# Performance work log

Measured on AMD Instinct MI355X. Metric: run time of the kernel, lower is better.

Reference implementation:

```python
import jax, jax.numpy as jnp
import numpy as np

LN_EPS = 1e-5


def setup_inputs() -> dict:
    key = jax.random.key(0)
    k1, k2, k3, k4 = jax.random.split(key, 4)
    N, D, E = 10000, 512, 150000
    scale = 1.0 / np.sqrt(D)
    return {
        "node_feature": jax.random.normal(k1, (N, D), dtype=jnp.float32),
        "edge_index": jax.random.randint(k2, (2, E), 0, N, dtype=jnp.int64),
        "ln_gamma": jnp.ones((D,), dtype=jnp.float32),
        "ln_beta": jnp.zeros((D,), dtype=jnp.float32),
        "w_l": jax.random.normal(k3, (D, D), dtype=jnp.float32) * scale,
        "b_l": jnp.zeros((D,), dtype=jnp.float32),
        "w_r": jax.random.normal(k4, (D, D), dtype=jnp.float32) * scale,
    }


def reference(node_feature, edge_index, ln_gamma, ln_beta, w_l, b_l, w_r):
    N = node_feature.shape[0]
    residual = node_feature

    # LayerNorm over feature dim
    mu = jnp.mean(node_feature, axis=-1, keepdims=True)
    var = jnp.mean(jnp.square(node_feature - mu), axis=-1, keepdims=True)
    x = (node_feature - mu) * jax.lax.rsqrt(var + LN_EPS) * ln_gamma + ln_beta

    # SAGEConv (mean aggr): gather x_j from src, segment-mean into dst
    src, dst = edge_index[0], edge_index[1]
    msg = x[src]                                   # [E, D]
    summed = jax.ops.segment_sum(msg, dst, num_segments=N)        # [N, D]
    cnt = jax.ops.segment_sum(jnp.ones_like(dst, dtype=x.dtype), dst, num_segments=N)
    agg = summed / jnp.maximum(cnt, 1.0)[:, None]

    # out = lin_l(agg) + lin_r(x)  (lin_r has no bias in PyG SAGEConv)
    out = agg @ w_l.T + b_l + x @ w_r.T
    out = jax.nn.relu(out)
    # dropout is identity in eval mode
    return out + residual
```

## Files before the change

### kernel.cpp

```cpp
#include <hip/hip_runtime.h>
#include <hip/hip_bf16.h>

typedef float f32x4 __attribute__((ext_vector_type(4)));
typedef __bf16 bf16x8 __attribute__((ext_vector_type(8)));
typedef unsigned short u16x8 __attribute__((ext_vector_type(8)));

#define N_NODES 10000
#define DIM 512
#define MPAD 10112
#define DEGCAP 96

__global__ __launch_bounds__(256) void zero_kernel(int* __restrict__ cnt) {
    cnt[blockIdx.x * 256 + threadIdx.x] = 0;
}

__global__ __launch_bounds__(256) void phase1_kernel(
    const float* __restrict__ wl, const float* __restrict__ wr,
    __hip_bfloat16* __restrict__ W,
    const float* __restrict__ xin, const float* __restrict__ gamma,
    const float* __restrict__ beta, __hip_bfloat16* __restrict__ A,
    const int* __restrict__ eidx, int* __restrict__ cnt, int* __restrict__ adj,
    int E, int fill_start) {
    int b = blockIdx.x;
    int tid = threadIdx.x;

    if (b < 512) {
        int idx = b * 256 + tid;
        int base = idx * 4;
        int d = base >> 10;
        int k = base & 1023;
        const float* src = (k < 512) ? (wl + d * 512 + k) : (wr + d * 512 + (k - 512));
        float4 v = *(const float4*)src;
        __hip_bfloat16* o = W + (size_t)d * 1024 + k;
        o[0] = __float2bfloat16(v.x);
        o[1] = __float2bfloat16(v.y);
        o[2] = __float2bfloat16(v.z);
        o[3] = __float2bfloat16(v.w);
    } else if (b < fill_start) {
        int row = (b - 512) * 4 + (tid >> 6);
        int lane = tid & 63;
        const float* xr = xin + (size_t)row * DIM + lane * 8;
        float4 v0 = *(const float4*)xr;
        float4 v1 = *(const float4*)(xr + 4);
        float s  = v0.x + v0.y + v0.z + v0.w + v1.x + v1.y + v1.z + v1.w;
        float ss = v0.x*v0.x + v0.y*v0.y + v0.z*v0.z + v0.w*v0.w
                 + v1.x*v1.x + v1.y*v1.y + v1.z*v1.z + v1.w*v1.w;
        #pragma unroll
        for (int o = 32; o > 0; o >>= 1) {
            s  += __shfl_xor(s, o, 64);
            ss += __shfl_xor(ss, o, 64);
        }
        float mu  = s * (1.0f / 512.0f);
        float var = ss * (1.0f / 512.0f) - mu * mu;
        float rstd = rsqrtf(var + 1e-5f);
        float4 g0 = *(const float4*)(gamma + lane * 8);
        float4 g1 = *(const float4*)(gamma + lane * 8 + 4);
        float4 b0 = *(const float4*)(beta + lane * 8);
        float4 b1 = *(const float4*)(beta + lane * 8 + 4);
        __hip_bfloat16* a = A + (size_t)row * 1024 + 512 + lane * 8;
        a[0] = __float2bfloat16((v0.x - mu) * rstd * g0.x + b0.x);
        a[1] = __float2bfloat16((v0.y - mu) * rstd * g0.y + b0.y);
        a[2] = __float2bfloat16((v0.z - mu) * rstd * g0.z + b0.z);
        a[3] = __float2bfloat16((v0.w - mu) * rstd * g0.w + b0.w);
        a[4] = __float2bfloat16((v1.x - mu) * rstd * g1.x + b1.x);
        a[5] = __float2bfloat16((v1.y - mu) * rstd * g1.y + b1.y);
        a[6] = __float2bfloat16((v1.z - mu) * rstd * g1.z + b1.z);
        a[7] = __float2bfloat16((v1.w - mu) * rstd * g1.w + b1.w);
    } else {
        int i = (b - fill_start) * 256 + tid;
        if (i < E) {
            int dst = eidx[E + i];
            int src = eidx[i];
            int pos = atomicAdd(&cnt[dst], 1);
            if (pos < DEGCAP) adj[dst * DEGCAP + pos] = src;
        }
    }
}

__global__ __launch_bounds__(256) void gather_kernel(const int* __restrict__ cnt,
                                                     const int* __restrict__ adj,
                                                     __hip_bfloat16* __restrict__ A) {
    int gw = (blockIdx.x * 256 + threadIdx.x) >> 6;
    int lane = threadIdx.x & 63;
    int deg = cnt[gw];
    const int* al = adj + gw * DEGCAP;
    float acc0[8] = {}, acc1[8] = {};
    int j = 0;
    for (; j + 8 <= deg; j += 8) {
        int a0 = al[j], a1 = al[j+1], a2 = al[j+2], a3 = al[j+3];
        int a4 = al[j+4], a5 = al[j+5], a6 = al[j+6], a7 = al[j+7];
        u16x8 v0 = *(const u16x8*)(A + (size_t)a0 * 1024 + 512 + lane * 8);
        u16x8 v1 = *(const u16x8*)(A + (size_t)a1 * 1024 + 512 + lane * 8);
        u16x8 v2 = *(const u16x8*)(A + (size_t)a2 * 1024 + 512 + lane * 8);
        u16x8 v3 = *(const u16x8*)(A + (size_t)a3 * 1024 + 512 + lane * 8);
        u16x8 v4 = *(const u16x8*)(A + (size_t)a4 * 1024 + 512 + lane * 8);
        u16x8 v5 = *(const u16x8*)(A + (size_t)a5 * 1024 + 512 + lane * 8);
        u16x8 v6 = *(const u16x8*)(A + (size_t)a6 * 1024 + 512 + lane * 8);
        u16x8 v7 = *(const u16x8*)(A + (size_t)a7 * 1024 + 512 + lane * 8);
        #pragma unroll
        for (int k = 0; k < 8; ++k) {
            acc0[k] += __uint_as_float((unsigned)v0[k] << 16)
                     + __uint_as_float((unsigned)v1[k] << 16)
                     + __uint_as_float((unsigned)v2[k] << 16)
                     + __uint_as_float((unsigned)v3[k] << 16);
            acc1[k] += __uint_as_float((unsigned)v4[k] << 16)
                     + __uint_as_float((unsigned)v5[k] << 16)
                     + __uint_as_float((unsigned)v6[k] << 16)
                     + __uint_as_float((unsigned)v7[k] << 16);
        }
    }
    for (; j + 4 <= deg; j += 4) {
        int a0 = al[j], a1 = al[j+1], a2 = al[j+2], a3 = al[j+3];
        u16x8 v0 = *(const u16x8*)(A + (size_t)a0 * 1024 + 512 + lane * 8);
        u16x8 v1 = *(const u16x8*)(A + (size_t)a1 * 1024 + 512 + lane * 8);
        u16x8 v2 = *(const u16x8*)(A + (size_t)a2 * 1024 + 512 + lane * 8);
        u16x8 v3 = *(const u16x8*)(A + (size_t)a3 * 1024 + 512 + lane * 8);
        #pragma unroll
        for (int k = 0; k < 8; ++k) {
            acc0[k] += __uint_as_float((unsigned)v0[k] << 16)
                     + __uint_as_float((unsigned)v1[k] << 16);
            acc1[k] += __uint_as_float((unsigned)v2[k] << 16)
                     + __uint_as_float((unsigned)v3[k] << 16);
        }
    }
    for (; j < deg; ++j) {
        int a0 = al[j];
        u16x8 v0 = *(const u16x8*)(A + (size_t)a0 * 1024 + 512 + lane * 8);
        #pragma unroll
        for (int k = 0; k < 8; ++k)
            acc0[k] += __uint_as_float((unsigned)v0[k] << 16);
    }
    float sc = 1.0f / fmaxf((float)deg, 1.0f);
    __hip_bfloat16* o = A + (size_t)gw * 1024 + lane * 8;
    #pragma unroll
    for (int k = 0; k < 8; ++k)
        o[k] = __float2bfloat16((acc0[k] + acc1[k]) * sc);
}

__global__ __launch_bounds__(256) void gemm_kernel(const __hip_bfloat16* __restrict__ A,
                                                   const __hip_bfloat16* __restrict__ Wb,
                                                   const float* __restrict__ bias,
                                                   const float* __restrict__ resid,
                                                   float* __restrict__ out) {
    __shared__ __hip_bfloat16 As[3][64 * 32];
    __shared__ __hip_bfloat16 Bs[3][64 * 32];
    const int tid = threadIdx.x;
    const int lane = tid & 63;
    const int w = tid >> 6;
    const int wr = w >> 1, wc = w & 1;

    int bid = blockIdx.x;
    int tl = (bid & 7) * 158 + (bid >> 3);
    int mx = tl >> 3, ny = tl & 7;
    const size_t arow0 = (size_t)mx * 64;
    const size_t bcol0 = (size_t)ny * 64;

    f32x4 acc[2][2] = {};

    const int rsw = ((lane & 15) >> 1) & 3;
    const int csw = (((lane >> 4) ^ rsw) & 3) * 8;

#define STAGE(buf, t)                                                                \
    {                                                                                \
        int r = tid >> 2, sl = tid & 3;                                              \
        int c8 = sl ^ ((r >> 1) & 3);                                                \
        const __hip_bfloat16* ga = A + (size_t)(arow0 + r) * 1024 + (t) * 32 + c8 * 8; \
        __builtin_amdgcn_global_load_lds(                                            \
            (const __attribute__((address_space(1))) void*)ga,                       \
            (__attribute__((address_space(3))) void*)(As[buf] + tid * 8), 16, 0, 0); \
        const __hip_bfloat16* gb = Wb + (size_t)(bcol0 + r) * 1024 + (t) * 32 + c8 * 8; \
        __builtin_amdgcn_global_load_lds(                                            \
            (const __attribute__((address_space(1))) void*)gb,                       \
            (__attribute__((address_space(3))) void*)(Bs[buf] + tid * 8), 16, 0, 0); \
    }

    STAGE(0, 0)
    STAGE(1, 1)

    #pragma unroll
    for (int t = 0; t < 32; ++t) {
        if (t < 31) { asm volatile("s_waitcnt vmcnt(2)" ::: "memory"); }
        else        { asm volatile("s_waitcnt vmcnt(0)" ::: "memory"); }
        __builtin_amdgcn_s_barrier();
        __builtin_amdgcn_sched_barrier(0);
        if (t + 2 < 32) STAGE((t + 2) % 3, t + 2)

        const int p = t % 3;
        bf16x8 af[2], bfr[2];
        #pragma unroll
        for (int m = 0; m < 2; ++m)
            af[m] = *(const bf16x8*)(As[p] + (wr * 32 + m * 16 + (lane & 15)) * 32 + csw);
        #pragma unroll
        for (int n = 0; n < 2; ++n)
            bfr[n] = *(const bf16x8*)(Bs[p] + (wc * 32 + n * 16 + (lane & 15)) * 32 + csw);
        #pragma unroll
        for (int m = 0; m < 2; ++m)
            #pragma unroll
            for (int n = 0; n < 2; ++n)
                acc[m][n] = __builtin_amdgcn_mfma_f32_16x16x32_bf16(af[m], bfr[n], acc[m][n], 0, 0, 0);
    }
#undef STAGE

    #pragma unroll
    for (int m = 0; m < 2; ++m) {
        int rowb = (int)arow0 + wr * 32 + m * 16 + (lane >> 4) * 4;
        #pragma unroll
        for (int n = 0; n < 2; ++n) {
            int col = (int)bcol0 + wc * 32 + n * 16 + (lane & 15);
            float bv = bias[col];
            #pragma unroll
            for (int j = 0; j < 4; ++j) {
                int row = rowb + j;
                if (row < N_NODES) {
                    float v = acc[m][n][j] + bv;
                    v = v > 0.0f ? v : 0.0f;
                    out[(size_t)row * 512 + col] = v + resid[(size_t)row * 512 + col];
                }
            }
        }
    }
}

extern "C" void kernel_launch(void* const* d_in, const int* in_sizes, int n_in,
                              void* d_out, int out_size, void* d_ws, size_t ws_size,
                              hipStream_t stream) {
    const float* node  = (const float*)d_in[0];
    const int*   eidx  = (const int*)d_in[1];
    const float* gamma = (const float*)d_in[2];
    const float* beta  = (const float*)d_in[3];
    const float* wl    = (const float*)d_in[4];
    const float* bl    = (const float*)d_in[5];
    const float* wr    = (const float*)d_in[6];
    float* out = (float*)d_out;
    const int E = in_sizes[1] / 2;

    char* ws = (char*)d_ws;
    int* cnt = (int*)ws;
    int* adj = cnt + 10240;
    size_t adj_bytes = ((size_t)N_NODES * DEGCAP * 4 + 255) & ~(size_t)255;
    __hip_bfloat16* A = (__hip_bfloat16*)((char*)adj + adj_bytes);
    __hip_bfloat16* W = (__hip_bfloat16*)((char*)A + (size_t)MPAD * 1024 * 2);

    const int fill_start = 512 + 2500;
    const int nFill = (E + 255) / 256;

    zero_kernel<<<40, 256, 0, stream>>>(cnt);
    phase1_kernel<<<fill_start + nFill, 256, 0, stream>>>(
        wl, wr, W, node, gamma, beta, A, eidx, cnt, adj, E, fill_start);
    gather_kernel<<<(N_NODES * 64) / 256, 256, 0, stream>>>(cnt, adj, A);
    gemm_kernel<<<1264, 256, 0, stream>>>(A, W, bl, node, out);
}
```

Measured before the change: 70.16 us.

## Partition gather feature columns by XCC with persistent atomic work queues

The gather kernel now reads the hardware XCC id and assigns each of four XCC groups a 128-column quarter of the normalized features. Blocks pull 4-node chunks from a per-quarter atomic queue, so each XCC's L2 only holds its own column slice of the feature table. The idea is to raise L2 hit rates for the random neighbour gathers and to balance uneven degrees through dynamic scheduling. In exchange each lane now does narrower 4-byte loads, each adjacency list is read four times, and the scheme relies on the XCC id mapping (xcc&3 on an 8-XCC part) and on an atomic counter per chunk.

```diff
diff --git a/kernel.cpp b/kernel.cpp
--- a/kernel.cpp
+++ b/kernel.cpp
@@ -79,62 +79,68 @@
 
 __global__ __launch_bounds__(256) void gather_kernel(const int* __restrict__ cnt,
                                                      const int* __restrict__ adj,
-                                                     __hip_bfloat16* __restrict__ A) {
-    int gw = (blockIdx.x * 256 + threadIdx.x) >> 6;
-    int lane = threadIdx.x & 63;
-    int deg = cnt[gw];
-    const int* al = adj + gw * DEGCAP;
-    float acc0[8] = {}, acc1[8] = {};
-    int j = 0;
-    for (; j + 8 <= deg; j += 8) {
-        int a0 = al[j], a1 = al[j+1], a2 = al[j+2], a3 = al[j+3];
-        int a4 = al[j+4], a5 = al[j+5], a6 = al[j+6], a7 = al[j+7];
-        u16x8 v0 = *(const u16x8*)(A + (size_t)a0 * 1024 + 512 + lane * 8);
-        u16x8 v1 = *(const u16x8*)(A + (size_t)a1 * 1024 + 512 + lane * 8);
-        u16x8 v2 = *(const u16x8*)(A + (size_t)a2 * 1024 + 512 + lane * 8);
-        u16x8 v3 = *(const u16x8*)(A + (size_t)a3 * 1024 + 512 + lane * 8);
-        u16x8 v4 = *(const u16x8*)(A + (size_t)a4 * 1024 + 512 + lane * 8);
-        u16x8 v5 = *(const u16x8*)(A + (size_t)a5 * 1024 + 512 + lane * 8);
-        u16x8 v6 = *(const u16x8*)(A + (size_t)a6 * 1024 + 512 + lane * 8);
-        u16x8 v7 = *(const u16x8*)(A + (size_t)a7 * 1024 + 512 + lane * 8);
-        #pragma unroll
-        for (int k = 0; k < 8; ++k) {
-            acc0[k] += __uint_as_float((unsigned)v0[k] << 16)
-                     + __uint_as_float((unsigned)v1[k] << 16)
-                     + __uint_as_float((unsigned)v2[k] << 16)
-                     + __uint_as_float((unsigned)v3[k] << 16);
-            acc1[k] += __uint_as_float((unsigned)v4[k] << 16)
-                     + __uint_as_float((unsigned)v5[k] << 16)
-                     + __uint_as_float((unsigned)v6[k] << 16)
-                     + __uint_as_float((unsigned)v7[k] << 16);
-        }
-    }
-    for (; j + 4 <= deg; j += 4) {
-        int a0 = al[j], a1 = al[j+1], a2 = al[j+2], a3 = al[j+3];
-        u16x8 v0 = *(const u16x8*)(A + (size_t)a0 * 1024 + 512 + lane * 8);
-        u16x8 v1 = *(const u16x8*)(A + (size_t)a1 * 1024 + 512 + lane * 8);
-        u16x8 v2 = *(const u16x8*)(A + (size_t)a2 * 1024 + 512 + lane * 8);
-        u16x8 v3 = *(const u16x8*)(A + (size_t)a3 * 1024 + 512 + lane * 8);
-        #pragma unroll
-        for (int k = 0; k < 8; ++k) {
-            acc0[k] += __uint_as_float((unsigned)v0[k] << 16)
-                     + __uint_as_float((unsigned)v1[k] << 16);
-            acc1[k] += __uint_as_float((unsigned)v2[k] << 16)
-                     + __uint_as_float((unsigned)v3[k] << 16);
-        }
-    }
-    for (; j < deg; ++j) {
-        int a0 = al[j];
-        u16x8 v0 = *(const u16x8*)(A + (size_t)a0 * 1024 + 512 + lane * 8);
-        #pragma unroll
-        for (int k = 0; k < 8; ++k)
-            acc0[k] += __uint_as_float((unsigned)v0[k] << 16);
-    }
-    float sc = 1.0f / fmaxf((float)deg, 1.0f);
-    __hip_bfloat16* o = A + (size_t)gw * 1024 + lane * 8;
-    #pragma unroll
-    for (int k = 0; k < 8; ++k)
-        o[k] = __float2bfloat16((acc0[k] + acc1[k]) * sc);
+                                                     __hip_bfloat16* __restrict__ A,
+                                                     int* __restrict__ queues) {
+    int xcc;
+    asm volatile("s_getreg_b32 %0, hwreg(HW_REG_XCC_ID)" : "=s"(xcc));
+    const int q = xcc & 3;
+    const int w = threadIdx.x >> 6;
+    const int lane = threadIdx.x & 63;
+    const char* xbase = (const char*)A + 1024 + (size_t)q * 256 + lane * 4;
+    __shared__ int chunk_s;
+
+    for (;;) {
+        if (threadIdx.x == 0) chunk_s = atomicAdd(&queues[q], 1);
+        __syncthreads();
+        int chunk = chunk_s;
+        __syncthreads();
+        if (chunk >= 2500) break;
+        int node = chunk * 4 + w;
+        int deg = cnt[node];
+        const int* al = adj + node * DEGCAP;
+        float a0 = 0.f, a1 = 0.f;
+        int j = 0;
+        for (; j + 8 <= deg; j += 8) {
+            int n0 = al[j],   n1 = al[j+1], n2 = al[j+2], n3 = al[j+3];
+            int n4 = al[j+4], n5 = al[j+5], n6 = al[j+6], n7 = al[j+7];
+            unsigned v0 = *(const unsigned*)(xbase + (size_t)n0 * 2048);
+            unsigned v1 = *(const unsigned*)(xbase + (size_t)n1 * 2048);
+            unsigned v2 = *(const unsigned*)(xbase + (size_t)n2 * 2048);
+            unsigned v3 = *(const unsigned*)(xbase + (size_t)n3 * 2048);
+            unsigned v4 = *(const unsigned*)(xbase + (size_t)n4 * 2048);
+            unsigned v5 = *(const unsigned*)(xbase + (size_t)n5 * 2048);
+            unsigned v6 = *(const unsigned*)(xbase + (size_t)n6 * 2048);
+            unsigned v7 = *(const unsigned*)(xbase + (size_t)n7 * 2048);
+            a0 += __uint_as_float(v0 << 16) + __uint_as_float(v1 << 16)
+                + __uint_as_float(v2 << 16) + __uint_as_float(v3 << 16)
+                + __uint_as_float(v4 << 16) + __uint_as_float(v5 << 16)
+                + __uint_as_float(v6 << 16) + __uint_as_float(v7 << 16);
+            a1 += __uint_as_float(v0 & 0xffff0000u) + __uint_as_float(v1 & 0xffff0000u)
+                + __uint_as_float(v2 & 0xffff0000u) + __uint_as_float(v3 & 0xffff0000u)
+                + __uint_as_float(v4 & 0xffff0000u) + __uint_as_float(v5 & 0xffff0000u)
+                + __uint_as_float(v6 & 0xffff0000u) + __uint_as_float(v7 & 0xffff0000u);
+        }
+        for (; j + 4 <= deg; j += 4) {
+            int n0 = al[j], n1 = al[j+1], n2 = al[j+2], n3 = al[j+3];
+            unsigned v0 = *(const unsigned*)(xbase + (size_t)n0 * 2048);
+            unsigned v1 = *(const unsigned*)(xbase + (size_t)n1 * 2048);
+            unsigned v2 = *(const unsigned*)(xbase + (size_t)n2 * 2048);
+            unsigned v3 = *(const unsigned*)(xbase + (size_t)n3 * 2048);
+            a0 += __uint_as_float(v0 << 16) + __uint_as_float(v1 << 16)
+                + __uint_as_float(v2 << 16) + __uint_as_float(v3 << 16);
+            a1 += __uint_as_float(v0 & 0xffff0000u) + __uint_as_float(v1 & 0xffff0000u)
+                + __uint_as_float(v2 & 0xffff0000u) + __uint_as_float(v3 & 0xffff0000u);
+        }
+        for (; j < deg; ++j) {
+            unsigned v0 = *(const unsigned*)(xbase + (size_t)al[j] * 2048);
+            a0 += __uint_as_float(v0 << 16);
+            a1 += __uint_as_float(v0 & 0xffff0000u);
+        }
+        float sc = 1.0f / fmaxf((float)deg, 1.0f);
+        __hip_bfloat16* o = (__hip_bfloat16*)((char*)A + (size_t)node * 2048 + (size_t)q * 256 + lane * 4);
+        o[0] = __float2bfloat16(a0 * sc);
+        o[1] = __float2bfloat16(a1 * sc);
+    }
 }
 
 __global__ __launch_bounds__(256) void gemm_kernel(const __hip_bfloat16* __restrict__ A,
@@ -235,8 +241,9 @@
     const int E = in_sizes[1] / 2;
 
     char* ws = (char*)d_ws;
-    int* cnt = (int*)ws;
-    int* adj = cnt + 10240;
+    int* cnt    = (int*)ws;
+    int* queues = cnt + 10240;
+    int* adj    = queues + 256;
     size_t adj_bytes = ((size_t)N_NODES * DEGCAP * 4 + 255) & ~(size_t)255;
     __hip_bfloat16* A = (__hip_bfloat16*)((char*)adj + adj_bytes);
     __hip_bfloat16* W = (__hip_bfloat16*)((char*)A + (size_t)MPAD * 1024 * 2);
@@ -244,9 +251,9 @@
     const int fill_start = 512 + 2500;
     const int nFill = (E + 255) / 256;
 
-    zero_kernel<<<40, 256, 0, stream>>>(cnt);
+    zero_kernel<<<41, 256, 0, stream>>>(cnt);
     phase1_kernel<<<fill_start + nFill, 256, 0, stream>>>(
         wl, wr, W, node, gamma, beta, A, eidx, cnt, adj, E, fill_start);
-    gather_kernel<<<(N_NODES * 64) / 256, 256, 0, stream>>>(cnt, adj, A);
+    gather_kernel<<<2048, 256, 0, stream>>>(cnt, adj, A, queues);
     gemm_kernel<<<1264, 256, 0, stream>>>(A, W, bl, node, out);
 }
```

Measured after the change: 191.2 us. +172.5%, slower.
